# Optimization experiments

Hardware: AMD Instinct MI355X
Metric: run time of the kernel (lower is better)

The kernel has to match this reference:

```python
import jax, jax.numpy as jnp
import numpy as np

B, D, K, L, H = 16384, 1024, 512, 128, 64  # batch, input_dim, num_components, latent_dim, phi hidden
EPS = 1e-9


def setup_inputs() -> dict:
    key = jax.random.key(0)
    k0, k1, k2, k3 = jax.random.split(key, 4)
    # small scales keep squared distances O(1-10) so exp(-d2) is non-degenerate
    x = jax.random.normal(k0, (B, D), jnp.float32) * 0.03
    z_samples = jax.random.normal(k1, (K, L), jnp.float32)
    W1 = jax.random.normal(k2, (L, H), jnp.float32) * (1.0 / np.sqrt(L)).astype(np.float32)
    b1 = jnp.zeros((H,), jnp.float32)
    W2 = jax.random.normal(k3, (H, D), jnp.float32) * 0.01
    b2 = jnp.zeros((D,), jnp.float32)
    return {"x": x, "z_samples": z_samples, "W1": W1, "b1": b1, "W2": W2, "b2": b2}


def reference(x, z_samples, W1, b1, W2, b2):
    # PhiNet: Linear -> ReLU -> Linear, applied to all components at once
    phi = jnp.maximum(z_samples @ W1 + b1, 0.0) @ W2 + b2          # (K, D)
    # ||x - phi_k||^2 for all (k, b) via GEMM expansion (fuses the per-component loop)
    sq = (jnp.sum(phi * phi, axis=-1)[:, None]
          + jnp.sum(x * x, axis=-1)[None, :]
          - 2.0 * (phi @ x.T))                                      # (K, B)
    lik = jnp.exp(-sq)                                              # (K, B)
    # weights = 1/K; sum_k w * lik = mean over K
    mixture_ll = jnp.log(jnp.mean(lik, axis=0) + EPS)               # (B,)
    return mixture_ll.mean()
```

## Files before the change

kernel.cpp:

```cpp
#include <hip/hip_runtime.h>
#include <hip/hip_bf16.h>
#include <stdint.h>

#define N_B   16384
#define D_DIM 1024
#define K_K   512
#define L_DIM 128
#define H_DIM 64

typedef __attribute__((ext_vector_type(8))) short short8;
typedef __attribute__((ext_vector_type(4))) float f32x4;

__device__ __forceinline__ unsigned short f2bf(float f) {
    union { float f; unsigned int u; } c; c.f = f;
    unsigned int u = c.u;
    unsigned int r = (u + 0x7FFFu + ((u >> 16) & 1u)) >> 16;
    return (unsigned short)r;
}
__device__ __forceinline__ float bf2f(unsigned short h) {
    union { unsigned int u; float f; } c; c.u = ((unsigned int)h) << 16;
    return c.f;
}

__global__ __launch_bounds__(256) void cvt_w2_kernel(const float* __restrict__ W2,
                                                     unsigned short* __restrict__ W2bf) {
    int i = blockIdx.x * 256 + threadIdx.x;
    const float4* src = (const float4*)W2;
    float4 v = src[i];
    ushort4 o;
    o.x = f2bf(v.x); o.y = f2bf(v.y); o.z = f2bf(v.z); o.w = f2bf(v.w);
    *(ushort4*)(W2bf + i * 4) = o;
}

__global__ __launch_bounds__(128) void prep_kernel(
    const float* __restrict__ z, const float* __restrict__ W1,
    const float* __restrict__ b1, const float* __restrict__ W2,
    const float* __restrict__ b2, unsigned short* __restrict__ h_bf,
    float* __restrict__ phi2) {
    __shared__ float zrow[4][L_DIM];
    __shared__ float hsh[4][H_DIM];
    __shared__ float redp[2][4];
    const int tid = threadIdx.x;
    const int kb = blockIdx.x * 4;
#pragma unroll
    for (int kk = 0; kk < 4; ++kk) zrow[kk][tid] = z[(kb + kk) * L_DIM + tid];
    __syncthreads();
    if (tid < H_DIM) {
        float bb = b1[tid];
        float s[4] = {bb, bb, bb, bb};
        for (int l = 0; l < L_DIM; ++l) {
            float w = W1[l * H_DIM + tid];
#pragma unroll
            for (int kk = 0; kk < 4; ++kk) s[kk] += zrow[kk][l] * w;
        }
#pragma unroll
        for (int kk = 0; kk < 4; ++kk) {
            float hv = fmaxf(s[kk], 0.0f);
            hsh[kk][tid] = hv;
            h_bf[(kb + kk) * H_DIM + tid] = f2bf(hv);
        }
    }
    __syncthreads();
    float ss[4] = {0.f, 0.f, 0.f, 0.f};
    for (int d = tid; d < D_DIM; d += 128) {
        float bb = b2[d];
        float a0 = bb, a1 = bb, a2 = bb, a3 = bb;
#pragma unroll
        for (int j = 0; j < H_DIM; ++j) {
            float w = W2[j * D_DIM + d];
            a0 += hsh[0][j] * w; a1 += hsh[1][j] * w;
            a2 += hsh[2][j] * w; a3 += hsh[3][j] * w;
        }
        ss[0] += a0 * a0; ss[1] += a1 * a1; ss[2] += a2 * a2; ss[3] += a3 * a3;
    }
    const int lane = tid & 63, wv = tid >> 6;
#pragma unroll
    for (int kk = 0; kk < 4; ++kk) {
        float v = ss[kk];
#pragma unroll
        for (int o = 1; o < 64; o <<= 1) v += __shfl_xor(v, o, 64);
        if (lane == 0) redp[wv][kk] = v;
    }
    __syncthreads();
    if (tid < 4) phi2[kb + tid] = redp[0][tid] + redp[1][tid];
}

__global__ __launch_bounds__(256) void main_kernel(
    const float* __restrict__ x, const unsigned short* __restrict__ W2bf,
    const unsigned short* __restrict__ h_bf, const float* __restrict__ phi2,
    const float* __restrict__ b2, float* __restrict__ lik_sum) {
    __shared__ float upart[4][32][H_DIM];
    __shared__ __align__(16) unsigned short u_tile[32 * H_DIM];
    __shared__ float phi2s[K_K];
    __shared__ __align__(16) float b2l[D_DIM];
    __shared__ float x2s[32], xb2s[32];
    __shared__ float red[4][32];

    const int tid = threadIdx.x;
    const int wv  = tid >> 6;
    const int l   = tid & 63;
    const int lm  = l & 15;
    const int q   = l >> 4;
    const int n0  = blockIdx.x * 32;

    phi2s[tid]       = phi2[tid];
    phi2s[256 + tid] = phi2[256 + tid];
    ((float4*)b2l)[tid] = ((const float4*)b2)[tid];
    if (tid < 32) { x2s[tid] = 0.f; xb2s[tid] = 0.f; }
    __syncthreads();

    f32x4 c1[2][4] = {};
    float x2p0 = 0.f, x2p1 = 0.f, xbp0 = 0.f, xbp1 = 0.f;
    const int dq = wv * 256;
#pragma unroll
    for (int s = 0; s < 8; ++s) {
        const int dl = dq + s * 32 + q * 8;
        float4 bb0 = *(const float4*)&b2l[dl];
        float4 bb1 = *(const float4*)&b2l[dl + 4];
        short8 af[2];
#pragma unroll
        for (int i = 0; i < 2; ++i) {
            const float* xp = x + (size_t)(n0 + i * 16 + lm) * D_DIM + dl;
            float4 v0 = *(const float4*)xp;
            float4 v1 = *(const float4*)(xp + 4);
            unsigned short u0 = f2bf(v0.x), u1 = f2bf(v0.y), u2 = f2bf(v0.z), u3 = f2bf(v0.w);
            unsigned short u4 = f2bf(v1.x), u5 = f2bf(v1.y), u6 = f2bf(v1.z), u7 = f2bf(v1.w);
            short8 a;
            a[0] = (short)u0; a[1] = (short)u1; a[2] = (short)u2; a[3] = (short)u3;
            a[4] = (short)u4; a[5] = (short)u5; a[6] = (short)u6; a[7] = (short)u7;
            af[i] = a;
            float f0 = bf2f(u0), f1 = bf2f(u1), f2 = bf2f(u2), f3 = bf2f(u3);
            float f4 = bf2f(u4), f5 = bf2f(u5), f6 = bf2f(u6), f7 = bf2f(u7);
            float s2 = f0*f0 + f1*f1 + f2*f2 + f3*f3 + f4*f4 + f5*f5 + f6*f6 + f7*f7;
            float sb = f0*bb0.x + f1*bb0.y + f2*bb0.z + f3*bb0.w
                     + f4*bb1.x + f5*bb1.y + f6*bb1.z + f7*bb1.w;
            if (i == 0) { x2p0 += s2; xbp0 += sb; } else { x2p1 += s2; xbp1 += sb; }
        }
        short8 bfr[4];
#pragma unroll
        for (int j = 0; j < 4; ++j)
            bfr[j] = *(const short8*)(W2bf + (size_t)(j * 16 + lm) * D_DIM + dl);
#pragma unroll
        for (int i = 0; i < 2; ++i)
#pragma unroll
            for (int j = 0; j < 4; ++j)
                c1[i][j] = __builtin_amdgcn_mfma_f32_16x16x32_bf16(af[i], bfr[j], c1[i][j], 0, 0, 0);
    }
#pragma unroll
    for (int i = 0; i < 2; ++i)
#pragma unroll
        for (int j = 0; j < 4; ++j)
#pragma unroll
            for (int r = 0; r < 4; ++r)
                upart[wv][i * 16 + q * 4 + r][j * 16 + lm] = c1[i][j][r];
    {
        float v0 = x2p0, v1 = x2p1, w0 = xbp0, w1 = xbp1;
        v0 += __shfl_xor(v0, 16, 64); v0 += __shfl_xor(v0, 32, 64);
        v1 += __shfl_xor(v1, 16, 64); v1 += __shfl_xor(v1, 32, 64);
        w0 += __shfl_xor(w0, 16, 64); w0 += __shfl_xor(w0, 32, 64);
        w1 += __shfl_xor(w1, 16, 64); w1 += __shfl_xor(w1, 32, 64);
        if (l < 16) {
            atomicAdd(&x2s[l], v0);       atomicAdd(&x2s[16 + l], v1);
            atomicAdd(&xb2s[l], w0);      atomicAdd(&xb2s[16 + l], w1);
        }
    }
    __syncthreads();
    const float* upf = &upart[0][0][0];
#pragma unroll
    for (int c = 0; c < 8; ++c) {
        int idx = c * 256 + tid;
        float sum = upf[idx] + upf[2048 + idx] + upf[4096 + idx] + upf[6144 + idx];
        u_tile[idx] = f2bf(sum);
    }
    __syncthreads();

    f32x4 acc[8][2] = {};
#pragma unroll
    for (int ks = 0; ks < 2; ++ks) {
        const int ko = ks * 32 + q * 8;
        short8 bfr[2];
#pragma unroll
        for (int j = 0; j < 2; ++j)
            bfr[j] = *(const short8*)&u_tile[(j * 16 + lm) * H_DIM + ko];
#pragma unroll
        for (int i = 0; i < 8; ++i) {
            short8 a = *(const short8*)(h_bf + (size_t)(wv * 128 + i * 16 + lm) * H_DIM + ko);
#pragma unroll
            for (int j = 0; j < 2; ++j)
                acc[i][j] = __builtin_amdgcn_mfma_f32_16x16x32_bf16(a, bfr[j], acc[i][j], 0, 0, 0);
        }
    }
    float xn0 = x2s[lm]      - 2.f * xb2s[lm];
    float xn1 = x2s[16 + lm] - 2.f * xb2s[16 + lm];
    float cs0 = 0.f, cs1 = 0.f;
#pragma unroll
    for (int i = 0; i < 8; ++i) {
#pragma unroll
        for (int r = 0; r < 4; ++r) {
            float p2 = phi2s[wv * 128 + i * 16 + q * 4 + r];
            cs0 += __expf(-(p2 + xn0 - 2.f * acc[i][0][r]));
            cs1 += __expf(-(p2 + xn1 - 2.f * acc[i][1][r]));
        }
    }
    cs0 += __shfl_xor(cs0, 16, 64); cs0 += __shfl_xor(cs0, 32, 64);
    cs1 += __shfl_xor(cs1, 16, 64); cs1 += __shfl_xor(cs1, 32, 64);
    if (l < 16) { red[wv][l] = cs0; red[wv][16 + l] = cs1; }
    __syncthreads();
    if (tid < 32)
        lik_sum[n0 + tid] = red[0][tid] + red[1][tid] + red[2][tid] + red[3][tid];
}

__global__ __launch_bounds__(1024) void reduce_kernel(const float* __restrict__ lik,
                                                      float* __restrict__ out) {
    const int tid = threadIdx.x;
    float s = 0.f;
#pragma unroll
    for (int c = 0; c < 16; ++c) {
        int b = c * 1024 + tid;
        s += __logf(lik[b] * (1.0f / (float)K_K) + 1e-9f);
    }
#pragma unroll
    for (int o = 1; o < 64; o <<= 1) s += __shfl_xor(s, o, 64);
    __shared__ float r[16];
    if ((tid & 63) == 0) r[tid >> 6] = s;
    __syncthreads();
    if (tid == 0) {
        float t = 0.f;
#pragma unroll
        for (int i = 0; i < 16; ++i) t += r[i];
        out[0] = t * (1.0f / (float)N_B);
    }
}

extern "C" void kernel_launch(void* const* d_in, const int* in_sizes, int n_in,
                              void* d_out, int out_size, void* d_ws, size_t ws_size,
                              hipStream_t stream) {
    const float* x  = (const float*)d_in[0];
    const float* z  = (const float*)d_in[1];
    const float* W1 = (const float*)d_in[2];
    const float* b1 = (const float*)d_in[3];
    const float* W2 = (const float*)d_in[4];
    const float* b2 = (const float*)d_in[5];

    char* ws = (char*)d_ws;
    unsigned short* W2bf   = (unsigned short*)(ws);
    unsigned short* h_bf   = (unsigned short*)(ws + 131072);
    float*          phi2   = (float*)(ws + 196608);
    float*          liks   = (float*)(ws + 200704);

    cvt_w2_kernel<<<64, 256, 0, stream>>>(W2, W2bf);
    prep_kernel<<<K_K / 4, 128, 0, stream>>>(z, W1, b1, W2, b2, h_bf, phi2);
    main_kernel<<<N_B / 32, 256, 0, stream>>>(x, W2bf, h_bf, phi2, b2, liks);
    reduce_kernel<<<1, 1024, 0, stream>>>(liks, (float*)d_out);
}
```

Measured before the change: 150.4 us.

## Fuse W2 conversion into prep, fold final log-reduce into main kernel, pad LDS

Merges the W2 bf16 conversion into the prep kernel, which now handles 8 components per block with 256 threads. The separate reduce kernel is removed: main computes the log per row, reduces within the block and atomically adds into the output after a memset. Shared-memory tiles are padded (68/72 strides) to cut bank conflicts, and bf16 packing uses the paired conversion intrinsic. The x-norm terms are now computed from fp32 x instead of the rounded bf16 values. Together these reduce launch count and per-element conversion cost, at the price of nondeterministic float atomics and a slight numerical change.

```diff
diff --git a/kernel.cpp b/kernel.cpp
--- a/kernel.cpp
+++ b/kernel.cpp
@@ -17,80 +17,85 @@
     unsigned int r = (u + 0x7FFFu + ((u >> 16) & 1u)) >> 16;
     return (unsigned short)r;
 }
-__device__ __forceinline__ float bf2f(unsigned short h) {
-    union { unsigned int u; float f; } c; c.u = ((unsigned int)h) << 16;
-    return c.f;
-}
-
-__global__ __launch_bounds__(256) void cvt_w2_kernel(const float* __restrict__ W2,
-                                                     unsigned short* __restrict__ W2bf) {
-    int i = blockIdx.x * 256 + threadIdx.x;
-    const float4* src = (const float4*)W2;
-    float4 v = src[i];
-    ushort4 o;
-    o.x = f2bf(v.x); o.y = f2bf(v.y); o.z = f2bf(v.z); o.w = f2bf(v.w);
-    *(ushort4*)(W2bf + i * 4) = o;
-}
-
-__global__ __launch_bounds__(128) void prep_kernel(
+
+__device__ __forceinline__ unsigned int pk2(float a, float b) {
+    __hip_bfloat162 t = __float22bfloat162_rn(make_float2(a, b));
+    union { __hip_bfloat162 h; unsigned int u; } c; c.h = t;
+    return c.u;
+}
+
+__global__ __launch_bounds__(256) void prep_kernel(
     const float* __restrict__ z, const float* __restrict__ W1,
     const float* __restrict__ b1, const float* __restrict__ W2,
-    const float* __restrict__ b2, unsigned short* __restrict__ h_bf,
-    float* __restrict__ phi2) {
-    __shared__ float zrow[4][L_DIM];
-    __shared__ float hsh[4][H_DIM];
-    __shared__ float redp[2][4];
+    const float* __restrict__ b2, unsigned short* __restrict__ W2bf,
+    unsigned short* __restrict__ h_bf, float* __restrict__ phi2) {
+    __shared__ float zsh[8][L_DIM];
+    __shared__ float hsh[8][H_DIM];
+    __shared__ float redp[4][8];
     const int tid = threadIdx.x;
-    const int kb = blockIdx.x * 4;
-#pragma unroll
-    for (int kk = 0; kk < 4; ++kk) zrow[kk][tid] = z[(kb + kk) * L_DIM + tid];
-    __syncthreads();
-    if (tid < H_DIM) {
-        float bb = b1[tid];
-        float s[4] = {bb, bb, bb, bb};
+    const int k0 = blockIdx.x * 8;
+
+    {
+        int i = blockIdx.x * 256 + tid;
+        float4 v = ((const float4*)W2)[i];
+        uint2 o = make_uint2(pk2(v.x, v.y), pk2(v.z, v.w));
+        *(uint2*)(W2bf + i * 4) = o;
+    }
+#pragma unroll
+    for (int c = 0; c < 4; ++c) {
+        int idx = c * 256 + tid;
+        zsh[idx >> 7][idx & 127] = z[k0 * L_DIM + idx];
+    }
+    __syncthreads();
+    {
+        const int j = tid & 63, kk = tid >> 6;
+        float bb = b1[j];
+        float s0 = bb, s1 = bb;
         for (int l = 0; l < L_DIM; ++l) {
-            float w = W1[l * H_DIM + tid];
-#pragma unroll
-            for (int kk = 0; kk < 4; ++kk) s[kk] += zrow[kk][l] * w;
-        }
-#pragma unroll
-        for (int kk = 0; kk < 4; ++kk) {
-            float hv = fmaxf(s[kk], 0.0f);
-            hsh[kk][tid] = hv;
-            h_bf[(kb + kk) * H_DIM + tid] = f2bf(hv);
-        }
-    }
-    __syncthreads();
-    float ss[4] = {0.f, 0.f, 0.f, 0.f};
-    for (int d = tid; d < D_DIM; d += 128) {
+            float w = W1[l * H_DIM + j];
+            s0 += zsh[kk][l] * w;
+            s1 += zsh[kk + 4][l] * w;
+        }
+        float h0 = fmaxf(s0, 0.0f), h1 = fmaxf(s1, 0.0f);
+        hsh[kk][j] = h0; hsh[kk + 4][j] = h1;
+        h_bf[(k0 + kk) * H_DIM + j]     = f2bf(h0);
+        h_bf[(k0 + kk + 4) * H_DIM + j] = f2bf(h1);
+    }
+    __syncthreads();
+    float ss[8] = {0.f, 0.f, 0.f, 0.f, 0.f, 0.f, 0.f, 0.f};
+#pragma unroll
+    for (int c = 0; c < 4; ++c) {
+        int d = c * 256 + tid;
         float bb = b2[d];
-        float a0 = bb, a1 = bb, a2 = bb, a3 = bb;
-#pragma unroll
+        float a[8];
+#pragma unroll
+        for (int kk = 0; kk < 8; ++kk) a[kk] = bb;
         for (int j = 0; j < H_DIM; ++j) {
             float w = W2[j * D_DIM + d];
-            a0 += hsh[0][j] * w; a1 += hsh[1][j] * w;
-            a2 += hsh[2][j] * w; a3 += hsh[3][j] * w;
-        }
-        ss[0] += a0 * a0; ss[1] += a1 * a1; ss[2] += a2 * a2; ss[3] += a3 * a3;
+#pragma unroll
+            for (int kk = 0; kk < 8; ++kk) a[kk] += hsh[kk][j] * w;
+        }
+#pragma unroll
+        for (int kk = 0; kk < 8; ++kk) ss[kk] += a[kk] * a[kk];
     }
     const int lane = tid & 63, wv = tid >> 6;
 #pragma unroll
-    for (int kk = 0; kk < 4; ++kk) {
+    for (int kk = 0; kk < 8; ++kk) {
         float v = ss[kk];
 #pragma unroll
         for (int o = 1; o < 64; o <<= 1) v += __shfl_xor(v, o, 64);
         if (lane == 0) redp[wv][kk] = v;
     }
     __syncthreads();
-    if (tid < 4) phi2[kb + tid] = redp[0][tid] + redp[1][tid];
+    if (tid < 8) phi2[k0 + tid] = redp[0][tid] + redp[1][tid] + redp[2][tid] + redp[3][tid];
 }
 
 __global__ __launch_bounds__(256) void main_kernel(
     const float* __restrict__ x, const unsigned short* __restrict__ W2bf,
     const unsigned short* __restrict__ h_bf, const float* __restrict__ phi2,
-    const float* __restrict__ b2, float* __restrict__ lik_sum) {
-    __shared__ float upart[4][32][H_DIM];
-    __shared__ __align__(16) unsigned short u_tile[32 * H_DIM];
+    const float* __restrict__ b2, float* __restrict__ out) {
+    __shared__ float upart[4][32][68];
+    __shared__ __align__(16) unsigned short u_tile[32 * 72];
     __shared__ float phi2s[K_K];
     __shared__ __align__(16) float b2l[D_DIM];
     __shared__ float x2s[32], xb2s[32];
@@ -123,17 +128,16 @@
             const float* xp = x + (size_t)(n0 + i * 16 + lm) * D_DIM + dl;
             float4 v0 = *(const float4*)xp;
             float4 v1 = *(const float4*)(xp + 4);
-            unsigned short u0 = f2bf(v0.x), u1 = f2bf(v0.y), u2 = f2bf(v0.z), u3 = f2bf(v0.w);
-            unsigned short u4 = f2bf(v1.x), u5 = f2bf(v1.y), u6 = f2bf(v1.z), u7 = f2bf(v1.w);
-            short8 a;
-            a[0] = (short)u0; a[1] = (short)u1; a[2] = (short)u2; a[3] = (short)u3;
-            a[4] = (short)u4; a[5] = (short)u5; a[6] = (short)u6; a[7] = (short)u7;
-            af[i] = a;
-            float f0 = bf2f(u0), f1 = bf2f(u1), f2 = bf2f(u2), f3 = bf2f(u3);
-            float f4 = bf2f(u4), f5 = bf2f(u5), f6 = bf2f(u6), f7 = bf2f(u7);
-            float s2 = f0*f0 + f1*f1 + f2*f2 + f3*f3 + f4*f4 + f5*f5 + f6*f6 + f7*f7;
-            float sb = f0*bb0.x + f1*bb0.y + f2*bb0.z + f3*bb0.w
-                     + f4*bb1.x + f5*bb1.y + f6*bb1.z + f7*bb1.w;
+            float s2 = v0.x*v0.x + v0.y*v0.y + v0.z*v0.z + v0.w*v0.w
+                     + v1.x*v1.x + v1.y*v1.y + v1.z*v1.z + v1.w*v1.w;
+            float sb = v0.x*bb0.x + v0.y*bb0.y + v0.z*bb0.z + v0.w*bb0.w
+                     + v1.x*bb1.x + v1.y*bb1.y + v1.z*bb1.z + v1.w*bb1.w;
+            union { short8 s8; unsigned int u[4]; } packu;
+            packu.u[0] = pk2(v0.x, v0.y);
+            packu.u[1] = pk2(v0.z, v0.w);
+            packu.u[2] = pk2(v1.x, v1.y);
+            packu.u[3] = pk2(v1.z, v1.w);
+            af[i] = packu.s8;
             if (i == 0) { x2p0 += s2; xbp0 += sb; } else { x2p1 += s2; xbp1 += sb; }
         }
         short8 bfr[4];
@@ -165,12 +169,13 @@
         }
     }
     __syncthreads();
-    const float* upf = &upart[0][0][0];
 #pragma unroll
     for (int c = 0; c < 8; ++c) {
         int idx = c * 256 + tid;
-        float sum = upf[idx] + upf[2048 + idx] + upf[4096 + idx] + upf[6144 + idx];
-        u_tile[idx] = f2bf(sum);
+        int row = idx >> 6, col = idx & 63;
+        float sum = upart[0][row][col] + upart[1][row][col]
+                  + upart[2][row][col] + upart[3][row][col];
+        u_tile[row * 72 + col] = f2bf(sum);
     }
     __syncthreads();
 
@@ -181,7 +186,7 @@
         short8 bfr[2];
 #pragma unroll
         for (int j = 0; j < 2; ++j)
-            bfr[j] = *(const short8*)&u_tile[(j * 16 + lm) * H_DIM + ko];
+            bfr[j] = *(const short8*)&u_tile[(j * 16 + lm) * 72 + ko];
 #pragma unroll
         for (int i = 0; i < 8; ++i) {
             short8 a = *(const short8*)(h_bf + (size_t)(wv * 128 + i * 16 + lm) * H_DIM + ko);
@@ -206,29 +211,15 @@
     cs1 += __shfl_xor(cs1, 16, 64); cs1 += __shfl_xor(cs1, 32, 64);
     if (l < 16) { red[wv][l] = cs0; red[wv][16 + l] = cs1; }
     __syncthreads();
-    if (tid < 32)
-        lik_sum[n0 + tid] = red[0][tid] + red[1][tid] + red[2][tid] + red[3][tid];
-}
-
-__global__ __launch_bounds__(1024) void reduce_kernel(const float* __restrict__ lik,
-                                                      float* __restrict__ out) {
-    const int tid = threadIdx.x;
-    float s = 0.f;
-#pragma unroll
-    for (int c = 0; c < 16; ++c) {
-        int b = c * 1024 + tid;
-        s += __logf(lik[b] * (1.0f / (float)K_K) + 1e-9f);
-    }
-#pragma unroll
-    for (int o = 1; o < 64; o <<= 1) s += __shfl_xor(s, o, 64);
-    __shared__ float r[16];
-    if ((tid & 63) == 0) r[tid >> 6] = s;
-    __syncthreads();
-    if (tid == 0) {
-        float t = 0.f;
-#pragma unroll
-        for (int i = 0; i < 16; ++i) t += r[i];
-        out[0] = t * (1.0f / (float)N_B);
+    if (tid < 32) {
+        float row_lik = red[0][tid] + red[1][tid] + red[2][tid] + red[3][tid];
+        float lg = __logf(row_lik * (1.0f / (float)K_K) + 1e-9f);
+        lg += __shfl_xor(lg, 1, 64);
+        lg += __shfl_xor(lg, 2, 64);
+        lg += __shfl_xor(lg, 4, 64);
+        lg += __shfl_xor(lg, 8, 64);
+        lg += __shfl_xor(lg, 16, 64);
+        if (tid == 0) atomicAdd(out, lg * (1.0f / (float)N_B));
     }
 }
 
@@ -243,13 +234,11 @@
     const float* b2 = (const float*)d_in[5];
 
     char* ws = (char*)d_ws;
-    unsigned short* W2bf   = (unsigned short*)(ws);
-    unsigned short* h_bf   = (unsigned short*)(ws + 131072);
-    float*          phi2   = (float*)(ws + 196608);
-    float*          liks   = (float*)(ws + 200704);
-
-    cvt_w2_kernel<<<64, 256, 0, stream>>>(W2, W2bf);
-    prep_kernel<<<K_K / 4, 128, 0, stream>>>(z, W1, b1, W2, b2, h_bf, phi2);
-    main_kernel<<<N_B / 32, 256, 0, stream>>>(x, W2bf, h_bf, phi2, b2, liks);
-    reduce_kernel<<<1, 1024, 0, stream>>>(liks, (float*)d_out);
-}
+    unsigned short* W2bf = (unsigned short*)(ws);
+    unsigned short* h_bf = (unsigned short*)(ws + 131072);
+    float*          phi2 = (float*)(ws + 196608);
+
+    hipMemsetAsync(d_out, 0, sizeof(float), stream);
+    prep_kernel<<<64, 256, 0, stream>>>(z, W1, b1, W2, b2, W2bf, h_bf, phi2);
+    main_kernel<<<N_B / 32, 256, 0, stream>>>(x, W2bf, h_bf, phi2, b2, (float*)d_out);
+}
```

Result: no change. 149.0 us (-1.0%).
